# Kernel optimization log

Hardware: AMD Instinct MI355X
Metric: run time of the kernel (lower is better)

## Reference

```python
import jax, jax.numpy as jnp
from jax import lax
import numpy as np

N, CIN, COUT, K, LAT, H = 8, 512, 512, 3, 512, 32
CINT = (CIN + COUT) // 2  # inter_channels
DN = ('NCHW', 'OIHW', 'NCHW')


def setup_inputs() -> dict:
    key = jax.random.key(0)
    ks = jax.random.split(key, 16)
    f = jax.random.normal
    return {
        'x': f(ks[0], (N, CIN, H, H), jnp.float32),
        'v': f(ks[1], (N, LAT), jnp.float32),
        'y': f(ks[2], (N, 3, H, H), jnp.float32),
        'noise1': f(ks[3], (N, 1, 2 * H, 2 * H), jnp.float32),
        'noise2': f(ks[4], (N, 1, 2 * H, 2 * H), jnp.float32),
        # Up_Mod_Conv: weight stored transposed -> [in, out, k, k]
        'up_w': f(ks[5], (CIN, CINT, K, K), jnp.float32) * 0.05,
        'up_b': f(ks[6], (CINT,), jnp.float32) * 0.05,
        'up_sw': f(ks[7], (LAT, CIN), jnp.float32) * 0.02,
        'up_sb': jnp.ones((CIN,), jnp.float32),
        # Modulated_Conv2d: weight [out, in, k, k]
        'c_w': f(ks[8], (COUT, CINT, K, K), jnp.float32) * 0.05,
        'c_b': f(ks[9], (COUT,), jnp.float32) * 0.05,
        'c_sw': f(ks[10], (LAT, CINT), jnp.float32) * 0.02,
        'c_sb': jnp.ones((CINT,), jnp.float32),
        # toRGB: 1x1, no demodulation
        'rgb_w': f(ks[11], (3, COUT, 1, 1), jnp.float32) * 0.05,
        'rgb_b': f(ks[12], (3,), jnp.float32) * 0.05,
        'rgb_sw': f(ks[13], (LAT, COUT), jnp.float32) * 0.02,
        'rgb_sb': jnp.ones((COUT,), jnp.float32),
        'noise_strength': jnp.full((1,), 0.1, jnp.float32),
    }


def _lrelu(x):
    return jnp.where(x > 0, x, 0.2 * x)  # LeakyReLU(0.2)


def _mod_conv(x, v, W, b, sw, sb, demod, pad):
    # Per-sample modulation s_i * W; since conv is linear this equals
    # conv(x * s) followed by per-sample/out-channel demod division.
    s = v @ sw + sb  # [N, Cin]
    out = lax.conv_general_dilated(x * s[:, :, None, None], W, (1, 1),
                                   ((pad, pad), (pad, pad)), dimension_numbers=DN)
    if demod:
        # sigma_no = sqrt(sum_{i,h,w} (s_ni * W_oihw)^2 + eps)
        sigma = jnp.sqrt(jnp.einsum('oihw,ni->no', W * W, s * s) + 1e-8)
        out = out / sigma[:, :, None, None]
    return out + b[None, :, None, None]


def _up_mod_conv(x, v, W, b, sw, sb):
    s = v @ sw + sb  # [N, Cin]
    Wt = jnp.flip(W, axis=(2, 3)).transpose(1, 0, 2, 3)  # [out, in, k, k]
    out = lax.conv_general_dilated(x * s[:, :, None, None], Wt, (1, 1),
                                   ((1, 2), (1, 2)), lhs_dilation=(2, 2),
                                   dimension_numbers=DN)
    # demod sums over in-channel dim and spatial dims of [in,out,k,k] weight
    sigma = jnp.sqrt(jnp.einsum('iohw,ni->no', W * W, s * s) + 1e-8)
    return out / sigma[:, :, None, None] + b[None, :, None, None]


def reference(x, v, y, noise1, noise2, up_w, up_b, up_sw, up_sb,
              c_w, c_b, c_sw, c_sb, rgb_w, rgb_b, rgb_sw, rgb_sb,
              noise_strength):
    h = _up_mod_conv(x, v, up_w, up_b, up_sw, up_sb)          # [N, CINT, 2H, 2H]
    h = _lrelu(h + noise_strength[0] * noise1)
    h = _mod_conv(h, v, c_w, c_b, c_sw, c_sb, True, K // 2)   # [N, COUT, 2H, 2H]
    h = _lrelu(h + noise_strength[0] * noise2)
    rgb = _lrelu(_mod_conv(h, v, rgb_w, rgb_b, rgb_sw, rgb_sb, False, 0))
    y_up = jax.image.resize(y, (y.shape[0], y.shape[1], 2 * y.shape[2], 2 * y.shape[3]),
                            method='bilinear')  # matches torch align_corners=False
    return (h, y_up + rgb)
```

## Files before the change

### kernel.cpp

```cpp
#include <hip/hip_runtime.h>
#include <hip/hip_bf16.h>

typedef unsigned short u16;
typedef u16  u16x4 __attribute__((ext_vector_type(4)));
typedef u16  u16x8 __attribute__((ext_vector_type(8)));
typedef __bf16 bf16;
typedef bf16 bf16x8 __attribute__((ext_vector_type(8)));
typedef float f32x4 __attribute__((ext_vector_type(4)));

__device__ __forceinline__ float b2f(u16 u){ return __uint_as_float(((unsigned)u)<<16); }
__device__ __forceinline__ u16 f2b(float f){ bf16 h = (bf16)f; return __builtin_bit_cast(u16, h); }
__device__ __forceinline__ float lrelu(float v){ return v > 0.f ? v : 0.2f*v; }

__device__ __forceinline__ void gll16(const u16* g, u16* l){
  __builtin_amdgcn_global_load_lds(
    (const __attribute__((address_space(1))) unsigned int*)(const void*)g,
    (__attribute__((address_space(3))) unsigned int*)(void*)l, 16, 0, 0);
}
#define VMCNT0() asm volatile("s_waitcnt vmcnt(0)" ::: "memory")
#define VMCNT4() asm volatile("s_waitcnt vmcnt(4)" ::: "memory")
#define BAR()    { asm volatile("" ::: "memory"); __builtin_amdgcn_s_barrier(); asm volatile("" ::: "memory"); }


__global__ __launch_bounds__(256) void prep_w_up(const float* __restrict__ up_w,
                                                 u16* __restrict__ Wup_t, float* __restrict__ wsq_up){
  const int t = blockIdx.x*256 + threadIdx.x;
  const int i = t & 511, o = t >> 9;
  const float* src = up_w + ((i<<9) + o)*9;
  float sq = 0.f;
  #pragma unroll
  for (int ky=0; ky<3; ++ky)
    #pragma unroll
    for (int kx=0; kx<3; ++kx){
      float w = src[ky*3+kx];
      sq += w*w;
      Wup_t[ (((2-ky)*3 + (2-kx))<<18) + (o<<9) + i ] = f2b(w);
    }
  wsq_up[(o<<9)+i] = sq;
}

__global__ __launch_bounds__(256) void prep_w_c(const float* __restrict__ c_w,
                                                u16* __restrict__ Wc_t, float* __restrict__ wsq_c){
  const int t = blockIdx.x*256 + threadIdx.x;
  const int i = t & 511, o = t >> 9;
  const float* src = c_w + ((o<<9) + i)*9;
  float sq = 0.f;
  #pragma unroll
  for (int tap=0; tap<9; ++tap){
    float w = src[tap];
    sq += w*w;
    Wc_t[ (tap<<18) + (o<<9) + i ] = f2b(w);
  }
  wsq_c[(o<<9)+i] = sq;
}

__global__ __launch_bounds__(256) void prep_s(const float* __restrict__ v,
    const float* __restrict__ up_sw, const float* __restrict__ up_sb,
    const float* __restrict__ c_sw,  const float* __restrict__ c_sb,
    const float* __restrict__ rgb_sw,const float* __restrict__ rgb_sb,
    float* __restrict__ s_up, float* __restrict__ s_c, float* __restrict__ s_rgb){
  const int t = blockIdx.x*256 + threadIdx.x;
  const int j = t & 511, n = t >> 9;
  const float* vn = v + (n<<9);
  float a=0.f, b=0.f, c=0.f;
  for (int l=0; l<512; ++l){
    float vl = vn[l];
    a += vl*up_sw[(l<<9)+j];
    b += vl*c_sw[(l<<9)+j];
    c += vl*rgb_sw[(l<<9)+j];
  }
  s_up[t] = a + up_sb[j];
  s_c[t]  = b + c_sb[j];
  s_rgb[t]= c + rgb_sb[j];
}

__global__ __launch_bounds__(256) void prep_sigma(const float* __restrict__ wsq_up, const float* __restrict__ wsq_c,
    const float* __restrict__ s_up, const float* __restrict__ s_c,
    float* __restrict__ sinv_up, float* __restrict__ sinv_c){
  const int t = blockIdx.x*256 + threadIdx.x;
  const int o = t & 511, n = t >> 9;
  const float* su = s_up + (n<<9);
  const float* sc = s_c  + (n<<9);
  const float* wu = wsq_up + (o<<9);
  const float* wc = wsq_c  + (o<<9);
  float au=0.f, ac=0.f;
  for (int l=0; l<512; ++l){
    float s1 = su[l]; au += wu[l]*s1*s1;
    float s2 = sc[l]; ac += wc[l]*s2*s2;
  }
  sinv_up[t] = 1.f/sqrtf(au + 1e-8f);
  sinv_c[t]  = 1.f/sqrtf(ac + 1e-8f);
}

__global__ __launch_bounds__(256) void fill_xp(const float* __restrict__ x,
    const float* __restrict__ s_up, u16* __restrict__ xp){
  const int b = blockIdx.x;
  const int n = b>>5, p = b&31;
  const int t = threadIdx.x;
  const int q = t&31, g = t>>5;
  const int cb = g<<6;
  #pragma unroll
  for (int j=0;j<8;++j){
    const int ch0 = cb + (j<<3);
    u16x8 pk;
    #pragma unroll
    for (int e=0;e<8;++e){
      float vv = x[ (((n<<9)+ch0+e)<<10) + (p<<5) + q ] * s_up[(n<<9)+ch0+e];
      pk[e] = f2b(vv);
    }
    *(u16x8*)&xp[ (((n*33+p)*36 + q)<<9) + ch0 ] = pk;
  }
}

__global__ __launch_bounds__(256, 2) void up_conv_k(
    const u16* __restrict__ xp, const u16* __restrict__ Wup_t,
    const float* __restrict__ sinv_up, const float* __restrict__ up_b,
    const float* __restrict__ s_c, const float* __restrict__ noise1,
    const float* __restrict__ nstr, u16* __restrict__ h1s)
{
  __shared__ __align__(16) u16 Bp[11520];
  __shared__ __align__(16) u16 Aa[2][8192];
  const int braw = blockIdx.x;
  const int bid = ((braw&7)<<7) | (braw>>3);
  const int og = bid & 3, tile = (bid>>2)&7, cls = (bid>>5)&3, n = bid>>7;
  const int cy = cls>>1, cx = cls&1;
  const int o0 = og<<7, r0 = tile<<2;
  const int tid = threadIdx.x;
  const int lane = tid & 63, wave = tid>>6;
  const int l15 = lane & 15, l4 = lane>>4;
  const int wm = wave>>1, wn = wave&1;
  const int xsw = l15 & 7;
  const int wub = tid & ~63;

  int wtap[4], dpl[4], dql[4]; int nt=0;
  for (int a = cy?0:1; a <= (cy?2:1); a += (cy?2:1))
    for (int b = cx?0:1; b <= (cx?2:1); b += (cx?2:1)){
      wtap[nt] = a*3+b; dpl[nt] = (cy+a-1)>>1; dql[nt] = (cx+b-1)>>1; ++nt;
    }

  f32x4 acc[4][4];
  #pragma unroll
  for (int i2=0;i2<4;++i2)
    #pragma unroll
    for (int j2=0;j2<4;++j2){ f32x4 z = {0.f,0.f,0.f,0.f}; acc[i2][j2]=z; }

  #pragma unroll 1
  for (int ci=0; ci<8; ++ci){
    const int i0 = ci<<6;
    #pragma unroll
    for (int k=0;k<6;++k){
      const int q = (k<<8) + tid;
      if (q < 1440){
        const int cell = q>>3, pc = q&7;
        const int rowl = cell/36, col = cell - rowl*36;
        const int cl = pc ^ (col&7);
        gll16(xp + (((n*33 + r0 + rowl)*36 + col)<<9) + i0 + (cl<<3),
              Bp + (((k<<8)+wub)<<3));
      }
    }
    #pragma unroll
    for (int k=0;k<4;++k){
      const int q = (k<<8) + tid;
      const int o = q>>3, pc = q&7;
      const int cl = pc ^ (o&7);
      gll16(Wup_t + (wtap[0]<<18) + ((o0+o)<<9) + i0 + (cl<<3),
            &Aa[0][ (((k<<8)+wub)<<3) ]);
    }
    VMCNT0();
    BAR();
    #pragma unroll 1
    for (int t=0; t<nt; ++t){
      const int dp = dpl[t], dq = dql[t];
      const int cur = t & 1;
      if (t+1 < nt){
        const int nxt = (t+1)&1;
        #pragma unroll
        for (int k=0;k<4;++k){
          const int q = (k<<8) + tid;
          const int o = q>>3, pc = q&7;
          const int cl = pc ^ (o&7);
          gll16(Wup_t + (wtap[t+1]<<18) + ((o0+o)<<9) + i0 + (cl<<3),
                &Aa[nxt][ (((k<<8)+wub)<<3) ]);
        }
        VMCNT4();
      } else {
        VMCNT0();
      }
      BAR();
      bf16x8 af[4][2], bfr[4][2];
      #pragma unroll
      for (int fm=0; fm<4; ++fm){
        const int o_r = (wm<<6)+(fm<<4)+l15;
        #pragma unroll
        for (int kh=0; kh<2; ++kh)
          af[fm][kh] = *(const bf16x8*)&Aa[cur][ (((o_r<<3) + (((kh<<2)+l4) ^ xsw))<<3) ];
      }
      #pragma unroll
      for (int fn=0; fn<4; ++fn){
        const int rr = (wn<<1) + (fn>>1), c = ((fn&1)<<4) + l15;
        const int row = rr + dp, col = c + dq;
        const int cell = row*36 + col, csw = col & 7;
        #pragma unroll
        for (int kh=0; kh<2; ++kh)
          bfr[fn][kh] = *(const bf16x8*)&Bp[ (((cell<<3) + (((kh<<2)+l4) ^ csw))<<3) ];
      }
      __builtin_amdgcn_s_setprio(1);
      #pragma unroll
      for (int kh=0; kh<2; ++kh)
        #pragma unroll
        for (int fm=0; fm<4; ++fm)
          #pragma unroll
          for (int fn=0; fn<4; ++fn)
            acc[fm][fn] = __builtin_amdgcn_mfma_f32_16x16x32_bf16(af[fm][kh], bfr[fn][kh], acc[fm][fn], 0,0,0);
      __builtin_amdgcn_s_setprio(0);
      BAR();
    }
  }
  const float ns = nstr[0];
  #pragma unroll
  for (int fm=0; fm<4; ++fm){
    const int oo0 = o0 + (wm<<6) + (fm<<4) + (l4<<2);
    float si[4], bb[4], sc2[4];
    #pragma unroll
    for (int r=0;r<4;++r){
      si[r] = sinv_up[(n<<9)+oo0+r];
      bb[r] = up_b[oo0+r];
      sc2[r]= s_c[(n<<9)+oo0+r];
    }
    #pragma unroll
    for (int fn=0; fn<4; ++fn){
      const int rr = (wn<<1) + (fn>>1), c = ((fn&1)<<4) + l15;
      const int Y = ((r0+rr)<<1) + cy, X = (c<<1) + cx;
      const float nz = ns * noise1[(n<<12) + (Y<<6) + X];
      u16x4 pk;
      #pragma unroll
      for (int r=0;r<4;++r){
        float v2 = acc[fm][fn][r]*si[r] + bb[r] + nz;
        pk[r] = f2b(lrelu(v2) * sc2[r]);
      }
      *(u16x4*)&h1s[ (((n*66 + Y+1)*66 + (X+1))<<9) + oo0 ] = pk;
    }
  }
}

__global__ __launch_bounds__(256, 2) void conv3x3_k(
    const u16* __restrict__ h1s, const u16* __restrict__ Wc_t,
    const float* __restrict__ sinv_c, const float* __restrict__ c_b,
    const float* __restrict__ noise2, const float* __restrict__ nstr,
    float* __restrict__ outh)
{
  __shared__ __align__(16) u16 Bp[16896];
  __shared__ __align__(16) u16 Aa[2][8192];
  const int braw = blockIdx.x;
  const int bid = ((braw&7)<<7) | (braw>>3);
  const int og = bid & 3, yp = (bid>>2)&31, n = bid>>7;
  const int o0 = og<<7, y0 = yp<<1;
  const int tid = threadIdx.x;
  const int lane = tid & 63, wave = tid>>6;
  const int l15 = lane & 15, l4 = lane>>4;
  const int wm = wave>>1, wn = wave&1;
  const int xsw = l15 & 7;
  const int wub = tid & ~63;

  f32x4 acc[4][4];
  #pragma unroll
  for (int i2=0;i2<4;++i2)
    #pragma unroll
    for (int j2=0;j2<4;++j2){ f32x4 z = {0.f,0.f,0.f,0.f}; acc[i2][j2]=z; }

  #pragma unroll 1
  for (int ci=0; ci<8; ++ci){
    const int i0 = ci<<6;
    #pragma unroll
    for (int k=0;k<9;++k){
      if (k==8 && tid>=64) continue;
      const int q = (k<<8) + tid;
      const int cell = q>>3, pc = q&7;
      const int row = cell/66, col = cell - row*66;
      const int cl = pc ^ (col&7);
      gll16(h1s + (((n*66 + y0 + row)*66 + col)<<9) + i0 + (cl<<3),
            Bp + (((k<<8)+wub)<<3));
    }
    #pragma unroll
    for (int k=0;k<4;++k){
      const int q = (k<<8) + tid;
      const int o = q>>3, pc = q&7;
      const int cl = pc ^ (o&7);
      gll16(Wc_t + ((o0+o)<<9) + i0 + (cl<<3),
            &Aa[0][ (((k<<8)+wub)<<3) ]);
    }
    VMCNT0();
    BAR();
    #pragma unroll 1
    for (int tap=0; tap<9; ++tap){
      const int ky = tap/3, kx = tap - ky*3;
      const int cur = tap & 1;
      if (tap < 8){
        const int nxt = (tap+1)&1;
        #pragma unroll
        for (int k=0;k<4;++k){
          const int q = (k<<8) + tid;
          const int o = q>>3, pc = q&7;
          const int cl = pc ^ (o&7);
          gll16(Wc_t + ((tap+1)<<18) + ((o0+o)<<9) + i0 + (cl<<3),
                &Aa[nxt][ (((k<<8)+wub)<<3) ]);
        }
        VMCNT4();
      } else {
        VMCNT0();
      }
      BAR();
      bf16x8 af[4][2], bfr[4][2];
      #pragma unroll
      for (int fm=0; fm<4; ++fm){
        const int o_r = (wm<<6)+(fm<<4)+l15;
        #pragma unroll
        for (int kh=0; kh<2; ++kh)
          af[fm][kh] = *(const bf16x8*)&Aa[cur][ (((o_r<<3) + (((kh<<2)+l4) ^ xsw))<<3) ];
      }
      #pragma unroll
      for (int fn=0; fn<4; ++fn){
        const int colx = (fn<<4) + l15 + kx;
        const int cell = (wn + ky)*66 + colx, csw = colx & 7;
        #pragma unroll
        for (int kh=0; kh<2; ++kh)
          bfr[fn][kh] = *(const bf16x8*)&Bp[ (((cell<<3) + (((kh<<2)+l4) ^ csw))<<3) ];
      }
      __builtin_amdgcn_s_setprio(1);
      #pragma unroll
      for (int kh=0; kh<2; ++kh)
        #pragma unroll
        for (int fm=0; fm<4; ++fm)
          #pragma unroll
          for (int fn=0; fn<4; ++fn)
            acc[fm][fn] = __builtin_amdgcn_mfma_f32_16x16x32_bf16(af[fm][kh], bfr[fn][kh], acc[fm][fn], 0,0,0);
      __builtin_amdgcn_s_setprio(0);
      BAR();
    }
  }
  const float ns = nstr[0];
  #pragma unroll
  for (int fm=0; fm<4; ++fm){
    #pragma unroll
    for (int r=0;r<4;++r){
      const int oo = o0 + (wm<<6)+(fm<<4)+(l4<<2)+r;
      const float si = sinv_c[(n<<9)+oo], bb = c_b[oo];
      #pragma unroll
      for (int fn=0; fn<4; ++fn){
        const int xq = (fn<<4)+l15;
        const int Y = y0 + wn;
        float v2 = acc[fm][fn][r]*si + bb + ns*noise2[(n<<12)+(Y<<6)+xq];
        outh[ (((n<<9)+oo)<<12) + (Y<<6) + xq ] = lrelu(v2);
      }
    }
  }
}

__global__ __launch_bounds__(256) void rgb_k(const float* __restrict__ h2,
    const float* __restrict__ s_rgb, const float* __restrict__ rgb_w, const float* __restrict__ rgb_b,
    const float* __restrict__ yin, float* __restrict__ out1)
{
  __shared__ float coef[3][512];
  __shared__ float part[4][3][64];
  const int braw = blockIdx.x;
  const int sb = ((braw&7)<<6) | (braw>>3);
  const int n = sb>>6, Y = sb&63;
  const int tid = threadIdx.x;
  for (int t = tid; t < 1536; t += 256){
    int c = t>>9, o = t&511;
    coef[c][o] = rgb_w[(c<<9)+o]*s_rgb[(n<<9)+o];
  }
  __syncthreads();
  const int wave = tid>>6, lane = tid&63;
  const float* base = h2 + ((size_t)(n<<9))*4096 + (Y<<6) + lane;
  float a0=0.f,a1=0.f,a2=0.f;
  for (int e=0;e<128;++e){
    int o = (wave<<7)+e;
    float h = base[(size_t)o<<12];
    a0 += h*coef[0][o]; a1 += h*coef[1][o]; a2 += h*coef[2][o];
  }
  part[wave][0][lane]=a0; part[wave][1][lane]=a1; part[wave][2][lane]=a2;
  __syncthreads();
  if (tid < 192){
    const int c = tid>>6, x2 = tid&63;
    float s = part[0][c][x2]+part[1][c][x2]+part[2][c][x2]+part[3][c][x2] + rgb_b[c];
    s = lrelu(s);
    float fy = 0.5f*Y - 0.25f, fx = 0.5f*x2 - 0.25f;
    int y0i = (int)floorf(fy); float wy = fy - y0i;
    int x0i = (int)floorf(fx); float wx = fx - x0i;
    int y0c = y0i<0?0:y0i, y1c = y0i+1>31?31:y0i+1;
    int x0c = x0i<0?0:x0i, x1c = x0i+1>31?31:x0i+1;
    const float* yb = yin + ((n*3 + c)<<10);
    float v00 = yb[(y0c<<5)+x0c], v01 = yb[(y0c<<5)+x1c];
    float v10 = yb[(y1c<<5)+x0c], v11 = yb[(y1c<<5)+x1c];
    float yup = (1.f-wy)*((1.f-wx)*v00 + wx*v01) + wy*((1.f-wx)*v10 + wx*v11);
    out1[ (((n*3+c)<<12)) + (Y<<6) + x2 ] = yup + s;
  }
}

extern "C" void kernel_launch(void* const* d_in, const int* in_sizes, int n_in,
                              void* d_out, int out_size, void* d_ws, size_t ws_size,
                              hipStream_t stream) {
  const float* x      = (const float*)d_in[0];
  const float* v      = (const float*)d_in[1];
  const float* yin    = (const float*)d_in[2];
  const float* noise1 = (const float*)d_in[3];
  const float* noise2 = (const float*)d_in[4];
  const float* up_w   = (const float*)d_in[5];
  const float* up_b   = (const float*)d_in[6];
  const float* up_sw  = (const float*)d_in[7];
  const float* up_sb  = (const float*)d_in[8];
  const float* c_w    = (const float*)d_in[9];
  const float* c_b    = (const float*)d_in[10];
  const float* c_sw   = (const float*)d_in[11];
  const float* c_sb   = (const float*)d_in[12];
  const float* rgb_w  = (const float*)d_in[13];
  const float* rgb_b  = (const float*)d_in[14];
  const float* rgb_sw = (const float*)d_in[15];
  const float* rgb_sb = (const float*)d_in[16];
  const float* nstr   = (const float*)d_in[17];

  char* w = (char*)d_ws;
  u16*   Wup_t  = (u16*)(w);
  u16*   Wc_t   = (u16*)(w + 4718592);
  float* wsq_up = (float*)(w + 9437184);
  float* wsq_c  = (float*)(w + 10485760);
  float* s_up   = (float*)(w + 11534336);
  float* s_c    = (float*)(w + 11550720);
  float* s_rgb  = (float*)(w + 11567104);
  float* sinv_up= (float*)(w + 11583488);
  float* sinv_c = (float*)(w + 11599872);
  u16*   xp     = (u16*)(w + 11616256);
  u16*   h1s    = (u16*)(w + 21348352);

  float* outh = (float*)d_out;
  float* out1 = (float*)d_out + 16777216;

  hipMemsetAsync(xp,  0, 9732096,  stream);
  hipMemsetAsync(h1s, 0, 35684352, stream);

  prep_w_up <<<1024, 256, 0, stream>>>(up_w, Wup_t, wsq_up);
  prep_w_c  <<<1024, 256, 0, stream>>>(c_w,  Wc_t,  wsq_c);
  prep_s    <<<16,   256, 0, stream>>>(v, up_sw, up_sb, c_sw, c_sb, rgb_sw, rgb_sb, s_up, s_c, s_rgb);
  prep_sigma<<<16,   256, 0, stream>>>(wsq_up, wsq_c, s_up, s_c, sinv_up, sinv_c);
  fill_xp   <<<256,  256, 0, stream>>>(x, s_up, xp);
  up_conv_k <<<1024, 256, 0, stream>>>(xp, Wup_t, sinv_up, up_b, s_c, noise1, nstr, h1s);
  conv3x3_k <<<1024, 256, 0, stream>>>(h1s, Wc_t, sinv_c, c_b, noise2, nstr, outh);
  rgb_k     <<<512,  256, 0, stream>>>(outh, s_rgb, rgb_w, rgb_b, yin, out1);
}
```

Measured before the change: 436.3 us.

## Stream activations from global into registers and triple-buffer weights per tap

Both conv kernels drop the LDS-staged activation tile. Each lane now loads its B fragments straight from global memory into registers, while weights go through a 3-slot LDS ring in a flattened (channel-block, tap) loop that prefetches one phase ahead with vmcnt-based waits. The full-buffer memsets are replaced by small kernels that zero only the padding ring of xp and h1s. This cuts LDS use and per-channel-block barriers and removes large memset traffic, at the cost of uncoalesced, repeated global reads for overlapping taps and higher register pressure.

After: 615.0 us. +40.9%, slower.

```diff
diff --git a/kernel.cpp b/kernel.cpp
--- a/kernel.cpp
+++ b/kernel.cpp
@@ -17,8 +17,7 @@
     (const __attribute__((address_space(1))) unsigned int*)(const void*)g,
     (__attribute__((address_space(3))) unsigned int*)(void*)l, 16, 0, 0);
 }
-#define VMCNT0() asm volatile("s_waitcnt vmcnt(0)" ::: "memory")
-#define VMCNT4() asm volatile("s_waitcnt vmcnt(4)" ::: "memory")
+#define VMCNTW(n) asm volatile("s_waitcnt vmcnt(" #n ")" ::: "memory")
 #define BAR()    { asm volatile("" ::: "memory"); __builtin_amdgcn_s_barrier(); asm volatile("" ::: "memory"); }
 
 
@@ -92,6 +91,32 @@
   sinv_c[t]  = 1.f/sqrtf(ac + 1e-8f);
 }
 
+__global__ __launch_bounds__(256) void zero_h1s_ring(u16* __restrict__ h1s){
+  const int t = blockIdx.x*256 + threadIdx.x;
+  const int chunk = t & 63;
+  const int cg = t >> 6;
+  const int n = cg / 260, c = cg - n*260;
+  int Y, X;
+  if (c < 66){ Y = 0; X = c; }
+  else if (c < 132){ Y = 65; X = c - 66; }
+  else if (c < 196){ Y = c - 131; X = 0; }
+  else { Y = c - 195; X = 65; }
+  u16x8 z = {0,0,0,0,0,0,0,0};
+  *(u16x8*)&h1s[ (size_t)(((n*66 + Y)*66 + X)<<9) + (chunk<<3) ] = z;
+}
+
+__global__ __launch_bounds__(256) void zero_xp_ring(u16* __restrict__ xp){
+  const int t = blockIdx.x*256 + threadIdx.x;
+  const int chunk = t & 63;
+  const int cg = t >> 6;
+  const int n = cg / 164, c = cg - n*164;
+  int p, q;
+  if (c < 128){ p = c >> 2; q = 32 + (c & 3); }
+  else { p = 32; q = c - 128; }
+  u16x8 z = {0,0,0,0,0,0,0,0};
+  *(u16x8*)&xp[ (size_t)(((n*33 + p)*36 + q)<<9) + (chunk<<3) ] = z;
+}
+
 __global__ __launch_bounds__(256) void fill_xp(const float* __restrict__ x,
     const float* __restrict__ s_up, u16* __restrict__ xp){
   const int b = blockIdx.x;
@@ -118,8 +143,7 @@
     const float* __restrict__ s_c, const float* __restrict__ noise1,
     const float* __restrict__ nstr, u16* __restrict__ h1s)
 {
-  __shared__ __align__(16) u16 Bp[11520];
-  __shared__ __align__(16) u16 Aa[2][8192];
+  __shared__ __align__(16) u16 Aa[24576];
   const int braw = blockIdx.x;
   const int bid = ((braw&7)<<7) | (braw>>3);
   const int og = bid & 3, tile = (bid>>2)&7, cls = (bid>>5)&3, n = bid>>7;
@@ -129,14 +153,10 @@
   const int lane = tid & 63, wave = tid>>6;
   const int l15 = lane & 15, l4 = lane>>4;
   const int wm = wave>>1, wn = wave&1;
-  const int xsw = l15 & 7;
   const int wub = tid & ~63;
-
-  int wtap[4], dpl[4], dql[4]; int nt=0;
-  for (int a = cy?0:1; a <= (cy?2:1); a += (cy?2:1))
-    for (int b = cx?0:1; b <= (cx?2:1); b += (cx?2:1)){
-      wtap[nt] = a*3+b; dpl[nt] = (cy+a-1)>>1; dql[nt] = (cx+b-1)>>1; ++nt;
-    }
+  const int nt = (cy?2:1)*(cx?2:1);
+  const int lg = (nt==4)?2:((nt==2)?1:0);
+  const int NPH = nt<<3;
 
   f32x4 acc[4][4];
   #pragma unroll
@@ -144,78 +164,75 @@
     #pragma unroll
     for (int j2=0;j2<4;++j2){ f32x4 z = {0.f,0.f,0.f,0.f}; acc[i2][j2]=z; }
 
-  #pragma unroll 1
-  for (int ci=0; ci<8; ++ci){
-    const int i0 = ci<<6;
-    #pragma unroll
-    for (int k=0;k<6;++k){
-      const int q = (k<<8) + tid;
-      if (q < 1440){
-        const int cell = q>>3, pc = q&7;
-        const int rowl = cell/36, col = cell - rowl*36;
-        const int cl = pc ^ (col&7);
-        gll16(xp + (((n*33 + r0 + rowl)*36 + col)<<9) + i0 + (cl<<3),
-              Bp + (((k<<8)+wub)<<3));
-      }
-    }
+  auto parms = [&](int p, int& tap, int& dp, int& dq, int& i0n){
+    const int ci_ = p >> lg, t = p & (nt-1);
+    const int ti = cx ? (t>>1) : t;
+    const int tj = cx ? (t&1) : 0;
+    const int a = cy ? (ti<<1) : 1;
+    const int b = cx ? (tj<<1) : 1;
+    tap = a*3 + b;
+    dp = (cy + a - 1) >> 1;
+    dq = (cx + b - 1) >> 1;
+    i0n = ci_ << 6;
+  };
+  auto issueA = [&](int pn){
+    int tap, dp, dq, i0n; parms(pn, tap, dp, dq, i0n);
+    const int bo = (pn % 3) << 13;
     #pragma unroll
     for (int k=0;k<4;++k){
       const int q = (k<<8) + tid;
       const int o = q>>3, pc = q&7;
       const int cl = pc ^ (o&7);
-      gll16(Wup_t + (wtap[0]<<18) + ((o0+o)<<9) + i0 + (cl<<3),
-            &Aa[0][ (((k<<8)+wub)<<3) ]);
-    }
-    VMCNT0();
+      gll16(Wup_t + (tap<<18) + ((o0+o)<<9) + i0n + (cl<<3),
+            Aa + bo + (((k<<8)+wub)<<3));
+    }
+  };
+  auto issueB = [&](int pn, u16x8 (&bn)[8]){
+    int tap, dp, dq, i0n; parms(pn, tap, dp, dq, i0n);
+    #pragma unroll
+    for (int fn=0; fn<4; ++fn){
+      const int rr = (wn<<1) + (fn>>1), c = ((fn&1)<<4) + l15;
+      const size_t cb = ((size_t)((n*33 + r0+rr+dp)*36 + (c+dq)) << 9) + i0n;
+      bn[fn*2+0] = *(const u16x8*)(xp + cb + (l4<<3));
+      bn[fn*2+1] = *(const u16x8*)(xp + cb + ((4+l4)<<3));
+    }
+  };
+  auto compute = [&](int p, u16x8 (&bc)[8]){
+    const u16* Ab = Aa + ((p % 3) << 13);
+    bf16x8 af[4][2];
+    #pragma unroll
+    for (int fm=0;fm<4;++fm){
+      const int o_r = (wm<<6)+(fm<<4)+l15;
+      #pragma unroll
+      for (int kh=0;kh<2;++kh)
+        af[fm][kh] = *(const bf16x8*)&Ab[ ((o_r<<3) + (((kh<<2)+l4) ^ (l15&7)))<<3 ];
+    }
+    __builtin_amdgcn_s_setprio(1);
+    #pragma unroll
+    for (int kh=0;kh<2;++kh)
+      #pragma unroll
+      for (int fm=0;fm<4;++fm)
+        #pragma unroll
+        for (int fn=0;fn<4;++fn)
+          acc[fm][fn] = __builtin_amdgcn_mfma_f32_16x16x32_bf16(
+              af[fm][kh], __builtin_bit_cast(bf16x8, bc[fn*2+kh]), acc[fm][fn], 0,0,0);
+    __builtin_amdgcn_s_setprio(0);
+  };
+
+  u16x8 bA[8], bB[8];
+  issueA(0); issueB(0, bA);
+  #pragma unroll 1
+  for (int pp=0; pp<NPH; pp+=2){
+    issueA(pp+1); issueB(pp+1, bB);
+    VMCNTW(12);
     BAR();
-    #pragma unroll 1
-    for (int t=0; t<nt; ++t){
-      const int dp = dpl[t], dq = dql[t];
-      const int cur = t & 1;
-      if (t+1 < nt){
-        const int nxt = (t+1)&1;
-        #pragma unroll
-        for (int k=0;k<4;++k){
-          const int q = (k<<8) + tid;
-          const int o = q>>3, pc = q&7;
-          const int cl = pc ^ (o&7);
-          gll16(Wup_t + (wtap[t+1]<<18) + ((o0+o)<<9) + i0 + (cl<<3),
-                &Aa[nxt][ (((k<<8)+wub)<<3) ]);
-        }
-        VMCNT4();
-      } else {
-        VMCNT0();
-      }
-      BAR();
-      bf16x8 af[4][2], bfr[4][2];
-      #pragma unroll
-      for (int fm=0; fm<4; ++fm){
-        const int o_r = (wm<<6)+(fm<<4)+l15;
-        #pragma unroll
-        for (int kh=0; kh<2; ++kh)
-          af[fm][kh] = *(const bf16x8*)&Aa[cur][ (((o_r<<3) + (((kh<<2)+l4) ^ xsw))<<3) ];
-      }
-      #pragma unroll
-      for (int fn=0; fn<4; ++fn){
-        const int rr = (wn<<1) + (fn>>1), c = ((fn&1)<<4) + l15;
-        const int row = rr + dp, col = c + dq;
-        const int cell = row*36 + col, csw = col & 7;
-        #pragma unroll
-        for (int kh=0; kh<2; ++kh)
-          bfr[fn][kh] = *(const bf16x8*)&Bp[ (((cell<<3) + (((kh<<2)+l4) ^ csw))<<3) ];
-      }
-      __builtin_amdgcn_s_setprio(1);
-      #pragma unroll
-      for (int kh=0; kh<2; ++kh)
-        #pragma unroll
-        for (int fm=0; fm<4; ++fm)
-          #pragma unroll
-          for (int fn=0; fn<4; ++fn)
-            acc[fm][fn] = __builtin_amdgcn_mfma_f32_16x16x32_bf16(af[fm][kh], bfr[fn][kh], acc[fm][fn], 0,0,0);
-      __builtin_amdgcn_s_setprio(0);
-      BAR();
-    }
-  }
+    compute(pp, bA);
+    if (pp+2 < NPH){ issueA(pp+2); issueB(pp+2, bA); VMCNTW(12); }
+    else { VMCNTW(0); }
+    BAR();
+    compute(pp+1, bB);
+  }
+
   const float ns = nstr[0];
   #pragma unroll
   for (int fm=0; fm<4; ++fm){
@@ -238,7 +255,7 @@
         float v2 = acc[fm][fn][r]*si[r] + bb[r] + nz;
         pk[r] = f2b(lrelu(v2) * sc2[r]);
       }
-      *(u16x4*)&h1s[ (((n*66 + Y+1)*66 + (X+1))<<9) + oo0 ] = pk;
+      *(u16x4*)&h1s[ (size_t)(((n*66 + Y+1)*66 + (X+1))<<9) + oo0 ] = pk;
     }
   }
 }
@@ -249,8 +266,7 @@
     const float* __restrict__ noise2, const float* __restrict__ nstr,
     float* __restrict__ outh)
 {
-  __shared__ __align__(16) u16 Bp[16896];
-  __shared__ __align__(16) u16 Aa[2][8192];
+  __shared__ __align__(16) u16 Aa[24576];
   const int braw = blockIdx.x;
   const int bid = ((braw&7)<<7) | (braw>>3);
   const int og = bid & 3, yp = (bid>>2)&31, n = bid>>7;
@@ -259,7 +275,6 @@
   const int lane = tid & 63, wave = tid>>6;
   const int l15 = lane & 15, l4 = lane>>4;
   const int wm = wave>>1, wn = wave&1;
-  const int xsw = l15 & 7;
   const int wub = tid & ~63;
 
   f32x4 acc[4][4];
@@ -268,76 +283,69 @@
     #pragma unroll
     for (int j2=0;j2<4;++j2){ f32x4 z = {0.f,0.f,0.f,0.f}; acc[i2][j2]=z; }
 
-  #pragma unroll 1
-  for (int ci=0; ci<8; ++ci){
-    const int i0 = ci<<6;
-    #pragma unroll
-    for (int k=0;k<9;++k){
-      if (k==8 && tid>=64) continue;
-      const int q = (k<<8) + tid;
-      const int cell = q>>3, pc = q&7;
-      const int row = cell/66, col = cell - row*66;
-      const int cl = pc ^ (col&7);
-      gll16(h1s + (((n*66 + y0 + row)*66 + col)<<9) + i0 + (cl<<3),
-            Bp + (((k<<8)+wub)<<3));
-    }
+  auto issueA = [&](int pn){
+    const int cin = (int)((unsigned)pn / 9u);
+    const int tapn = pn - cin*9;
+    const int i0n = cin << 6;
+    const int bo = (pn % 3) << 13;
     #pragma unroll
     for (int k=0;k<4;++k){
       const int q = (k<<8) + tid;
       const int o = q>>3, pc = q&7;
       const int cl = pc ^ (o&7);
-      gll16(Wc_t + ((o0+o)<<9) + i0 + (cl<<3),
-            &Aa[0][ (((k<<8)+wub)<<3) ]);
-    }
-    VMCNT0();
+      gll16(Wc_t + (tapn<<18) + ((o0+o)<<9) + i0n + (cl<<3),
+            Aa + bo + (((k<<8)+wub)<<3));
+    }
+  };
+  auto issueB = [&](int pn, u16x8 (&bn)[8]){
+    const int cin = (int)((unsigned)pn / 9u);
+    const int tapn = pn - cin*9;
+    const int kyn = tapn/3, kxn = tapn - kyn*3;
+    const int i0n = cin << 6;
+    #pragma unroll
+    for (int fn=0; fn<4; ++fn){
+      const int colx = (fn<<4) + l15 + kxn;
+      const size_t cb = ((size_t)((n*66 + y0+wn+kyn)*66 + colx) << 9) + i0n;
+      bn[fn*2+0] = *(const u16x8*)(h1s + cb + (l4<<3));
+      bn[fn*2+1] = *(const u16x8*)(h1s + cb + ((4+l4)<<3));
+    }
+  };
+  auto compute = [&](int p, u16x8 (&bc)[8]){
+    const u16* Ab = Aa + ((p % 3) << 13);
+    bf16x8 af[4][2];
+    #pragma unroll
+    for (int fm=0;fm<4;++fm){
+      const int o_r = (wm<<6)+(fm<<4)+l15;
+      #pragma unroll
+      for (int kh=0;kh<2;++kh)
+        af[fm][kh] = *(const bf16x8*)&Ab[ ((o_r<<3) + (((kh<<2)+l4) ^ (l15&7)))<<3 ];
+    }
+    __builtin_amdgcn_s_setprio(1);
+    #pragma unroll
+    for (int kh=0;kh<2;++kh)
+      #pragma unroll
+      for (int fm=0;fm<4;++fm)
+        #pragma unroll
+        for (int fn=0;fn<4;++fn)
+          acc[fm][fn] = __builtin_amdgcn_mfma_f32_16x16x32_bf16(
+              af[fm][kh], __builtin_bit_cast(bf16x8, bc[fn*2+kh]), acc[fm][fn], 0,0,0);
+    __builtin_amdgcn_s_setprio(0);
+  };
+
+  u16x8 bA[8], bB[8];
+  issueA(0); issueB(0, bA);
+  #pragma unroll 1
+  for (int pp=0; pp<72; pp+=2){
+    issueA(pp+1); issueB(pp+1, bB);
+    VMCNTW(12);
     BAR();
-    #pragma unroll 1
-    for (int tap=0; tap<9; ++tap){
-      const int ky = tap/3, kx = tap - ky*3;
-      const int cur = tap & 1;
-      if (tap < 8){
-        const int nxt = (tap+1)&1;
-        #pragma unroll
-        for (int k=0;k<4;++k){
-          const int q = (k<<8) + tid;
-          const int o = q>>3, pc = q&7;
-          const int cl = pc ^ (o&7);
-          gll16(Wc_t + ((tap+1)<<18) + ((o0+o)<<9) + i0 + (cl<<3),
-                &Aa[nxt][ (((k<<8)+wub)<<3) ]);
-        }
-        VMCNT4();
-      } else {
-        VMCNT0();
-      }
-      BAR();
-      bf16x8 af[4][2], bfr[4][2];
-      #pragma unroll
-      for (int fm=0; fm<4; ++fm){
-        const int o_r = (wm<<6)+(fm<<4)+l15;
-        #pragma unroll
-        for (int kh=0; kh<2; ++kh)
-          af[fm][kh] = *(const bf16x8*)&Aa[cur][ (((o_r<<3) + (((kh<<2)+l4) ^ xsw))<<3) ];
-      }
-      #pragma unroll
-      for (int fn=0; fn<4; ++fn){
-        const int colx = (fn<<4) + l15 + kx;
-        const int cell = (wn + ky)*66 + colx, csw = colx & 7;
-        #pragma unroll
-        for (int kh=0; kh<2; ++kh)
-          bfr[fn][kh] = *(const bf16x8*)&Bp[ (((cell<<3) + (((kh<<2)+l4) ^ csw))<<3) ];
-      }
-      __builtin_amdgcn_s_setprio(1);
-      #pragma unroll
-      for (int kh=0; kh<2; ++kh)
-        #pragma unroll
-        for (int fm=0; fm<4; ++fm)
-          #pragma unroll
-          for (int fn=0; fn<4; ++fn)
-            acc[fm][fn] = __builtin_amdgcn_mfma_f32_16x16x32_bf16(af[fm][kh], bfr[fn][kh], acc[fm][fn], 0,0,0);
-      __builtin_amdgcn_s_setprio(0);
-      BAR();
-    }
-  }
+    compute(pp, bA);
+    if (pp+2 < 72){ issueA(pp+2); issueB(pp+2, bA); VMCNTW(12); }
+    else { VMCNTW(0); }
+    BAR();
+    compute(pp+1, bB);
+  }
+
   const float ns = nstr[0];
   #pragma unroll
   for (int fm=0; fm<4; ++fm){
@@ -350,7 +358,7 @@
         const int xq = (fn<<4)+l15;
         const int Y = y0 + wn;
         float v2 = acc[fm][fn][r]*si + bb + ns*noise2[(n<<12)+(Y<<6)+xq];
-        outh[ (((n<<9)+oo)<<12) + (Y<<6) + xq ] = lrelu(v2);
+        outh[ (size_t)(((n<<9)+oo)<<12) + (Y<<6) + xq ] = lrelu(v2);
       }
     }
   }
@@ -436,15 +444,14 @@
   float* outh = (float*)d_out;
   float* out1 = (float*)d_out + 16777216;
 
-  hipMemsetAsync(xp,  0, 9732096,  stream);
-  hipMemsetAsync(h1s, 0, 35684352, stream);
-
-  prep_w_up <<<1024, 256, 0, stream>>>(up_w, Wup_t, wsq_up);
-  prep_w_c  <<<1024, 256, 0, stream>>>(c_w,  Wc_t,  wsq_c);
-  prep_s    <<<16,   256, 0, stream>>>(v, up_sw, up_sb, c_sw, c_sb, rgb_sw, rgb_sb, s_up, s_c, s_rgb);
-  prep_sigma<<<16,   256, 0, stream>>>(wsq_up, wsq_c, s_up, s_c, sinv_up, sinv_c);
-  fill_xp   <<<256,  256, 0, stream>>>(x, s_up, xp);
-  up_conv_k <<<1024, 256, 0, stream>>>(xp, Wup_t, sinv_up, up_b, s_c, noise1, nstr, h1s);
-  conv3x3_k <<<1024, 256, 0, stream>>>(h1s, Wc_t, sinv_c, c_b, noise2, nstr, outh);
-  rgb_k     <<<512,  256, 0, stream>>>(outh, s_rgb, rgb_w, rgb_b, yin, out1);
-}
+  prep_w_up    <<<1024, 256, 0, stream>>>(up_w, Wup_t, wsq_up);
+  prep_w_c     <<<1024, 256, 0, stream>>>(c_w,  Wc_t,  wsq_c);
+  prep_s       <<<16,   256, 0, stream>>>(v, up_sw, up_sb, c_sw, c_sb, rgb_sw, rgb_sb, s_up, s_c, s_rgb);
+  prep_sigma   <<<16,   256, 0, stream>>>(wsq_up, wsq_c, s_up, s_c, sinv_up, sinv_c);
+  zero_xp_ring <<<328,  256, 0, stream>>>(xp);
+  zero_h1s_ring<<<520,  256, 0, stream>>>(h1s);
+  fill_xp      <<<256,  256, 0, stream>>>(x, s_up, xp);
+  up_conv_k    <<<1024, 256, 0, stream>>>(xp, Wup_t, sinv_up, up_b, s_c, noise1, nstr, h1s);
+  conv3x3_k    <<<1024, 256, 0, stream>>>(h1s, Wc_t, sinv_c, c_b, noise2, nstr, outh);
+  rgb_k        <<<512,  256, 0, stream>>>(outh, s_rgb, rgb_w, rgb_b, yin, out1);
+}
```
